# Kernel optimization log

Hardware: AMD Instinct MI355X
Metric: run time of the kernel (lower is better)

The kernel has to match this reference:

```python
import jax, jax.numpy as jnp
import numpy as np
from jax import lax

B, C, D, H, W = 2, 256, 32, 64, 192
TRAIN_W = 640
DISPS = np.arange(D, dtype=np.float32) * 0.01  # norm_disp_range


def conv1x1(x, w, b):
    # x [B,Cin,H,W], w [Cout,Cin]
    return jnp.einsum('bchw,oc->bohw', x, w) + b[None, :, None, None]


def conv3x3(x, w, b):
    y = lax.conv_general_dilated(x, w, (1, 1), 'SAME',
                                 dimension_numbers=('NCHW', 'OIHW', 'NCHW'))
    return y + b[None, :, None, None]


def warp_volume(x, shift_px):
    """Horizontal bilinear warp with border clamp for each disparity.
    x [B,Cc,H,W], shift_px [B,D] (pixel shift) -> [B,Cc,D,H,W]."""
    Wd = x.shape[3]
    j = jnp.arange(Wd, dtype=x.dtype)
    src = jnp.clip(j[None, None, :] + shift_px[:, :, None], 0.0, Wd - 1.0)  # [B,D,W]
    x0 = jnp.floor(src).astype(jnp.int32)
    x1 = jnp.minimum(x0 + 1, Wd - 1)
    frac = src - x0.astype(src.dtype)  # [B,D,W]

    def one(xb, i0, i1, fb):
        g0 = xb[:, :, i0]  # [Cc,H,D,W]
        g1 = xb[:, :, i1]
        out = g0 * (1.0 - fb) + g1 * fb
        return out.transpose(0, 2, 1, 3)  # [Cc,D,H,W]

    return jax.vmap(one)(x, x0, x1, frac)


def setup_inputs() -> dict:
    key = jax.random.key(0)
    ks = jax.random.split(key, 16)
    f32 = jnp.float32
    inp = {
        't_feat': jax.random.normal(ks[0], (B, C, H, W), f32),
        's_feat': jax.random.normal(ks[1], (B, C, H, W), f32),
        'directs': jnp.ones((B, 1, 1, 1), f32),
        'qw': jax.random.normal(ks[2], (C // 4, C), f32) * 0.05,
        'qb': jax.random.normal(ks[3], (C // 4,), f32) * 0.05,
        'kw': jax.random.normal(ks[4], (C // 4, C), f32) * 0.05,
        'kb': jax.random.normal(ks[5], (C // 4,), f32) * 0.05,
        'vw': jax.random.normal(ks[6], (C // 4, C), f32) * 0.05,
        'vb': jax.random.normal(ks[7], (C // 4,), f32) * 0.05,
        'p1w': jax.random.normal(ks[8], (C // 4, C // 2, 3, 3), f32) * 0.05,
        'p1b': jax.random.normal(ks[9], (C // 4,), f32) * 0.05,
        'p2w': jax.random.normal(ks[10], (D, C // 4, 3, 3), f32) * 0.05,
        'p2b': jax.random.normal(ks[11], (D,), f32) * 0.05,
        'rw': jax.random.normal(ks[12], (C, C + D), f32) * 0.05,
        'rb': jax.random.normal(ks[13], (C,), f32) * 0.05,
        'img_w': TRAIN_W,
    }
    return inp


def reference(t_feat, s_feat, directs, qw, qb, kw, kb, vw, vb,
              p1w, p1b, p2w, p2b, rw, rb, img_w):
    rel_scale = (TRAIN_W / img_w) if img_w != TRAIN_W else 1.0
    q = conv1x1(t_feat, qw, qb)  # [B,C/4,H,W]
    k = conv1x1(s_feat, kw, kb)
    v = conv1x1(s_feat, vw, vb)

    Wd = t_feat.shape[3]
    disps = jnp.asarray(DISPS, t_feat.dtype)
    # normalized shift d*2*rel_scale*directs -> pixels: * (W-1)/2
    shift = disps[None, :] * rel_scale * directs.reshape(-1, 1) * (Wd - 1)  # [B,D]

    wk = warp_volume(k, shift)  # [B,C/4,D,H,W]
    wv = warp_volume(v, shift)

    cq = q.shape[1]
    cost = jnp.einsum('bchw,bcdhw->bdhw', q, wk) / (cq ** 0.5)  # [B,D,H,W]
    norm_cost = jax.nn.softmax(cost, axis=1)
    agg_v = jnp.einsum('bdhw,bcdhw->bchw', norm_cost, wv)  # [B,C/4,H,W]

    h1 = jax.nn.elu(conv3x3(jnp.concatenate([q, agg_v], axis=1), p1w, p1b))
    res_cost = conv3x3(h1, p2w, p2b)  # [B,D,H,W]
    cost = (cost + res_cost) * 0.5
    norm_cost = jax.nn.softmax(cost, axis=1)
    x = jax.nn.elu(conv1x1(jnp.concatenate([t_feat, norm_cost], axis=1), rw, rb))
    return x, cost
```

## Files before the change

kernel.cpp:

```cpp
#include <hip/hip_runtime.h>

#define BB 2
#define CC 256
#define CQ 64
#define DD 32
#define HH 64
#define WW 192
#define HW (HH*WW)
#define NPIX (BB*HW)

typedef __attribute__((ext_vector_type(8))) short bf16x8;
typedef __attribute__((ext_vector_type(4))) float f32x4;

__device__ __forceinline__ float b2f(ushort s){ return __uint_as_float(((uint)s)<<16); }
__device__ __forceinline__ ushort f2b(float f){
    uint u = __float_as_uint(f);
    return (ushort)((u + 0x7fffu + ((u>>16)&1u)) >> 16);
}
__device__ __forceinline__ float eluf(float v){ return v > 0.f ? v : (__expf(v)-1.f); }

__global__ __launch_bounds__(256) void k_prep_w(
    const float* __restrict__ qw, const float* __restrict__ qb,
    const float* __restrict__ kw, const float* __restrict__ kb,
    const float* __restrict__ vw, const float* __restrict__ vb,
    const float* __restrict__ p1w, const float* __restrict__ p2w,
    const float* __restrict__ rw,
    ushort* __restrict__ Wqkv, float* __restrict__ bqkv,
    ushort* __restrict__ A1, ushort* __restrict__ A2, ushort* __restrict__ Ar)
{
    int id = blockIdx.x*256 + threadIdx.x;
    if (id < 49152) {
        int o = id / 256, c = id % 256;
        float v = (o<64)? qw[o*256+c] : (o<128)? kw[(o-64)*256+c] : vw[(o-128)*256+c];
        Wqkv[id] = f2b(v);
    } else if (id < 49344) {
        int o = id - 49152;
        bqkv[o] = (o<64)? qb[o] : (o<128)? kb[o-64] : vb[o-128];
    } else if (id < 49344+73728) {
        int i = id - 49344;
        int o = i/1152, r = i%1152, t = r/128, ci = r%128;
        A1[i] = f2b(p1w[(size_t)(o*128+ci)*9 + t]);
    } else if (id < 49344+73728+18432) {
        int i = id - (49344+73728);
        int o = i/576, r = i%576, t = r/64, ci = r%64;
        A2[i] = f2b(p2w[(size_t)(o*64+ci)*9 + t]);
    } else if (id < 49344+73728+18432+73728) {
        int i = id - (49344+73728+18432);
        Ar[i] = f2b(rw[i]);
    }
}

__global__ __launch_bounds__(256) void g_qkv(
    const float* __restrict__ t_feat, const float* __restrict__ s_feat,
    const ushort* __restrict__ Wqkv, const float* __restrict__ bqkv,
    ushort* __restrict__ X1, ushort* __restrict__ VbT)
{
    __shared__ ushort sT[32*264];
    __shared__ ushort sS[32*264];
    int tid = threadIdx.x;
    int bid = blockIdx.x;
    int tile = (bid & 7)*96 + (bid >> 3);
    int p0 = tile * 32;
    int b0  = p0 / HW;
    int pl0 = p0 % HW;

    for (int i = tid; i < 1024; i += 256){
        int px = i & 31, c8 = i >> 5;
        const float* pt = t_feat + ((size_t)(b0*CC + c8*8))*HW + pl0 + px;
        const float* ps = s_feat + ((size_t)(b0*CC + c8*8))*HW + pl0 + px;
        uint ut[4], us[4];
        #pragma unroll
        for (int j2=0;j2<4;++j2){
            ut[j2] = (uint)f2b(pt[(size_t)(2*j2)*HW]) | ((uint)f2b(pt[(size_t)(2*j2+1)*HW])<<16);
            us[j2] = (uint)f2b(ps[(size_t)(2*j2)*HW]) | ((uint)f2b(ps[(size_t)(2*j2+1)*HW])<<16);
        }
        uint4 qt; qt.x=ut[0]; qt.y=ut[1]; qt.z=ut[2]; qt.w=ut[3];
        uint4 qs; qs.x=us[0]; qs.y=us[1]; qs.z=us[2]; qs.w=us[3];
        *(uint4*)&sT[(px*33 + c8)*8] = qt;
        *(uint4*)&sS[(px*33 + c8)*8] = qs;
    }
    __syncthreads();

    int wv = tid >> 6, lane = tid & 63;
    int lm = lane & 15, lk = lane >> 4;
    f32x4 acc[3][2];
    #pragma unroll
    for (int g=0;g<3;++g){ acc[g][0]=(f32x4){0.f,0.f,0.f,0.f}; acc[g][1]=(f32x4){0.f,0.f,0.f,0.f}; }
    const ushort* Ap = Wqkv + (size_t)(wv*16 + lm)*CC + lk*8;

    #pragma unroll
    for (int k0=0; k0<CC; k0+=32){
        bf16x8 a0 = *(const bf16x8*)(Ap + k0);
        bf16x8 a1 = *(const bf16x8*)(Ap + 64*CC + k0);
        bf16x8 a2 = *(const bf16x8*)(Ap + 128*CC + k0);
        #pragma unroll
        for (int nt=0; nt<2; ++nt){
            int ch = (nt*16+lm)*33 + (k0>>3) + lk;
            bf16x8 bT = *(const bf16x8*)&sT[ch*8];
            bf16x8 bS = *(const bf16x8*)&sS[ch*8];
            acc[0][nt] = __builtin_amdgcn_mfma_f32_16x16x32_bf16(a0, bT, acc[0][nt], 0,0,0);
            acc[1][nt] = __builtin_amdgcn_mfma_f32_16x16x32_bf16(a1, bS, acc[1][nt], 0,0,0);
            acc[2][nt] = __builtin_amdgcn_mfma_f32_16x16x32_bf16(a2, bS, acc[2][nt], 0,0,0);
        }
    }
    int ol = wv*16 + lk*4;
    #pragma unroll
    for (int nt=0; nt<2; ++nt){
        int p = p0 + nt*16 + lm;
        {
            int ob = ol;
            uint u0 = (uint)f2b(acc[0][nt][0]+bqkv[ob])   | ((uint)f2b(acc[0][nt][1]+bqkv[ob+1])<<16);
            uint u1 = (uint)f2b(acc[0][nt][2]+bqkv[ob+2]) | ((uint)f2b(acc[0][nt][3]+bqkv[ob+3])<<16);
            *(uint2*)(X1 + (size_t)p*128 + ol) = make_uint2(u0, u1);
        }
        {
            int ob = 64 + ol;
            uint u0 = (uint)f2b(acc[1][nt][0]+bqkv[ob])   | ((uint)f2b(acc[1][nt][1]+bqkv[ob+1])<<16);
            uint u1 = (uint)f2b(acc[1][nt][2]+bqkv[ob+2]) | ((uint)f2b(acc[1][nt][3]+bqkv[ob+3])<<16);
            *(uint2*)(X1 + (size_t)p*128 + 64 + ol) = make_uint2(u0, u1);
        }
        #pragma unroll
        for (int j=0;j<4;++j)
            VbT[(size_t)(ol+j)*NPIX + p] = f2b(acc[2][nt][j] + bqkv[128 + ol + j]);
    }
}

#define BANDC 96
#define STS 36
#define PFS 100
#define VTS2 104
__global__ __launch_bounds__(512) void k_ca(
    const ushort* __restrict__ X1, const ushort* __restrict__ VbT,
    const float* __restrict__ directs, const int* __restrict__ img_w_p,
    float* __restrict__ C1, ushort* __restrict__ Agg)
{
    __shared__ float  sF[BANDC*STS];
    __shared__ ushort sPC[32*VTS2];
    int tid = threadIdx.x;
    int j   = blockIdx.x;
    int r8  = j & 7;
    int kk  = j >> 3;
    int sub = kk % 6;
    int rhi = kk / 6;
    int row = rhi*8 + r8;
    int b   = row >> 6;
    int h   = row & 63;
    int w0  = sub * 32;
    size_t rowbase = (size_t)b*HW + (size_t)h*WW;

    int imw = img_w_p[0];
    float rel = (imw != 640) ? (640.0f/(float)imw) : 1.0f;
    float sf = 0.01f * rel * directs[b] * 191.0f;
    int bl = (sf < 0.f) ? (w0 - 64) : w0;

    int w8 = tid >> 6, lane = tid & 63;
    int lm = lane & 15, lk = lane >> 4;

    {
        int mt = w8 & 1;
        int q  = w0 + mt*16 + lm;
        const ushort* Qp = X1 + (rowbase + q)*128 + lk*8;
        bf16x8 aq0 = *(const bf16x8*)(Qp);
        bf16x8 aq1 = *(const bf16x8*)(Qp + 32);
        for (int nt = (w8 >> 1); nt < 6; nt += 4){
            int xrow = nt*16 + lm;
            int gx = bl + xrow;
            bf16x8 b0 = {0,0,0,0,0,0,0,0}, b1 = {0,0,0,0,0,0,0,0};
            if (gx >= 0 && gx < WW){
                const ushort* Kp = X1 + (rowbase + gx)*128 + 64 + lk*8;
                b0 = *(const bf16x8*)(Kp);
                b1 = *(const bf16x8*)(Kp + 32);
            }
            f32x4 acc = {0.f,0.f,0.f,0.f};
            acc = __builtin_amdgcn_mfma_f32_16x16x32_bf16(aq0, b0, acc, 0,0,0);
            acc = __builtin_amdgcn_mfma_f32_16x16x32_bf16(aq1, b1, acc, 0,0,0);
            *(f32x4*)&sF[xrow*STS + mt*16 + lk*4] = acc;
        }
    }
    __syncthreads();

    int px  = tid >> 4;
    int l16 = tid & 15;
    int w   = w0 + px;
    size_t n = rowbase + w;
    float wf = (float)w;

    float cost[2]; int xi0[2], xi1[2]; float frk[2];
    #pragma unroll
    for (int t=0; t<2; ++t){
        int d = l16*2 + t;
        float srcx = fminf(fmaxf(wf + (float)d*sf, 0.f), 191.0f);
        int x0 = (int)floorf(srcx);
        int x1 = min(x0+1, WW-1);
        float fr = srcx - (float)x0;
        int i0 = min(max(x0 - bl, 0), BANDC-1);
        int i1 = min(max(x1 - bl, 0), BANDC-1);
        xi0[t] = i0; xi1[t] = i1; frk[t] = fr;
        float s0 = sF[i0*STS + px];
        float s1 = sF[i1*STS + px];
        cost[t] = (s0 + fr*(s1-s0)) * 0.125f;
    }
    *(float2*)(C1 + n*DD + l16*2) = make_float2(cost[0], cost[1]);
    float mm = fmaxf(cost[0], cost[1]);
    mm = fmaxf(mm, __shfl_xor(mm, 1));
    mm = fmaxf(mm, __shfl_xor(mm, 2));
    mm = fmaxf(mm, __shfl_xor(mm, 4));
    mm = fmaxf(mm, __shfl_xor(mm, 8));
    float e0 = __expf(cost[0]-mm), e1 = __expf(cost[1]-mm);
    float ss = e0 + e1;
    ss += __shfl_xor(ss, 1);
    ss += __shfl_xor(ss, 2);
    ss += __shfl_xor(ss, 4);
    ss += __shfl_xor(ss, 8);
    float inv = 1.f/ss;
    float p0 = e0*inv, p1 = e1*inv;
    __syncthreads();

    for (int i = tid; i < (32*PFS)/4; i += 512)
        *(f32x4*)&sF[i*4] = (f32x4){0.f,0.f,0.f,0.f};
    __syncthreads();

    {
        float w1a = p0*frk[0], w0a = p0 - w1a;
        float w1b = p1*frk[1], w0b = p1 - w1b;
        atomicAdd(&sF[px*PFS + xi0[0]], w0a);
        atomicAdd(&sF[px*PFS + xi1[0]], w1a);
        atomicAdd(&sF[px*PFS + xi0[1]], w0b);
        atomicAdd(&sF[px*PFS + xi1[1]], w1b);
    }
    __syncthreads();

    {
        int base = l16*6;
        #pragma unroll
        for (int q=0; q<3; ++q){
            float2 v2 = *(const float2*)&sF[px*PFS + base + q*2];
            *(uint*)&sPC[px*VTS2 + base + q*2] = (uint)f2b(v2.x) | ((uint)f2b(v2.y)<<16);
        }
    }
    __syncthreads();

    {
        int mi = w8 & 3;
        int ni = w8 >> 2;
        int c  = mi*16 + lm;
        int wr = ni*16 + lm;
        const ushort* Vp = VbT + (size_t)c*NPIX + rowbase + bl;
        f32x4 acc = {0.f,0.f,0.f,0.f};
        #pragma unroll
        for (int kt=0; kt<3; ++kt){
            int gx = bl + kt*32 + lk*8;
            bf16x8 a = {0,0,0,0,0,0,0,0};
            if (gx >= 0 && gx < WW) a = *(const bf16x8*)(Vp + kt*32 + lk*8);
            bf16x8 bbf = *(const bf16x8*)&sPC[wr*VTS2 + kt*32 + lk*8];
            acc = __builtin_amdgcn_mfma_f32_16x16x32_bf16(a, bbf, acc, 0,0,0);
        }
        uint u0 = (uint)f2b(acc[0]) | ((uint)f2b(acc[1])<<16);
        uint u1 = (uint)f2b(acc[2]) | ((uint)f2b(acc[3])<<16);
        *(uint2*)(Agg + (rowbase + w0 + wr)*64 + mi*16 + lk*4) = make_uint2(u0, u1);
    }
}

__global__ __launch_bounds__(256) void g_conv1(
    const ushort* __restrict__ X1, const ushort* __restrict__ Agg,
    const ushort* __restrict__ A1, const float* __restrict__ p1b,
    ushort* __restrict__ X2)
{
    __shared__ ushort sB[3*16*34*8];
    int tid = threadIdx.x;
    int wv = tid >> 6, lane = tid & 63;
    int lm = lane & 15, lk = lane >> 4;
    int bid = blockIdx.x;
    int tile = (bid & 7)*96 + (bid >> 3);
    int n0 = tile * 32;
    int b  = n0 / HW;
    int pl = n0 % HW;
    int h  = pl / WW, w0 = pl % WW;

    for (int i = tid; i < 1632; i += 256){
        int dh = i / 544, rem2 = i % 544;
        int c16 = rem2 / 34, x = rem2 % 34;
        int hh = h + dh - 1, wx = w0 + x - 1;
        uint4 val = make_uint4(0,0,0,0);
        if (hh >= 0 && hh < HH && wx >= 0 && wx < WW){
            size_t pix = (size_t)b*HW + (size_t)hh*WW + wx;
            val = (c16 < 8) ? *(const uint4*)(X1 + pix*128 + c16*8)
                            : *(const uint4*)(Agg + pix*64 + (c16-8)*8);
        }
        *(uint4*)&sB[((dh*16 + c16)*34 + x)*8] = val;
    }
    __syncthreads();

    int mw = wv & 1, nw = wv >> 1;
    const ushort* Ap = A1 + (size_t)(mw*32 + lm)*1152 + lk*8;
    f32x4 acc0 = {0.f,0.f,0.f,0.f}, acc1 = {0.f,0.f,0.f,0.f};
    int xb = nw*16 + lm;
    #pragma unroll
    for (int t=0; t<9; ++t){
        int dh = t/3, dw = t%3;
        #pragma unroll
        for (int c0=0; c0<128; c0+=32){
            bf16x8 bb = *(const bf16x8*)&sB[((dh*16 + (c0>>3)+lk)*34 + xb + dw)*8];
            bf16x8 a0 = *(const bf16x8*)(Ap + t*128 + c0);
            bf16x8 a1 = *(const bf16x8*)(Ap + (size_t)16*1152 + t*128 + c0);
            acc0 = __builtin_amdgcn_mfma_f32_16x16x32_bf16(a0, bb, acc0, 0,0,0);
            acc1 = __builtin_amdgcn_mfma_f32_16x16x32_bf16(a1, bb, acc1, 0,0,0);
        }
    }
    int pg = n0 + nw*16 + lm;
    int o0 = mw*32 + lk*4;
    {
        uint u0 = (uint)f2b(eluf(acc0[0]+p1b[o0]))   | ((uint)f2b(eluf(acc0[1]+p1b[o0+1]))<<16);
        uint u1 = (uint)f2b(eluf(acc0[2]+p1b[o0+2])) | ((uint)f2b(eluf(acc0[3]+p1b[o0+3]))<<16);
        *(uint2*)(X2 + (size_t)pg*64 + o0) = make_uint2(u0, u1);
        int o1 = o0 + 16;
        uint u2 = (uint)f2b(eluf(acc1[0]+p1b[o1]))   | ((uint)f2b(eluf(acc1[1]+p1b[o1+1]))<<16);
        uint u3 = (uint)f2b(eluf(acc1[2]+p1b[o1+2])) | ((uint)f2b(eluf(acc1[3]+p1b[o1+3]))<<16);
        *(uint2*)(X2 + (size_t)pg*64 + o1) = make_uint2(u2, u3);
    }
}

__global__ __launch_bounds__(256) void g_conv2final(
    const ushort* __restrict__ X2, const ushort* __restrict__ A2,
    const float* __restrict__ p2b, const float* __restrict__ C1,
    const float* __restrict__ t_feat, const ushort* __restrict__ Ar,
    const float* __restrict__ rb,
    float* __restrict__ cost_out, float* __restrict__ xout)
{
    __shared__ ushort sT[32*264];
    __shared__ float  sO[32*36];
    __shared__ ushort sN[32*40];
    ushort* sB = sT;
    int tid = threadIdx.x;
    int wv = tid >> 6, lane = tid & 63;
    int lm = lane & 15, lk = lane >> 4;
    int bid = blockIdx.x;
    int tile = (bid & 7)*96 + (bid >> 3);
    int n0 = tile * 32;
    int b  = n0 / HW;
    int pl = n0 % HW;
    int h  = pl / WW, w0 = pl % WW;

    for (int i = tid; i < 816; i += 256){
        int dh = i / 272, rem2 = i % 272;
        int c16 = rem2 / 34, x = rem2 % 34;
        int hh = h + dh - 1, wx = w0 + x - 1;
        uint4 val = make_uint4(0,0,0,0);
        if (hh >= 0 && hh < HH && wx >= 0 && wx < WW)
            val = *(const uint4*)(X2 + ((size_t)b*HW + (size_t)hh*WW + wx)*64 + c16*8);
        *(uint4*)&sB[((dh*8 + c16)*34 + x)*8] = val;
    }
    __syncthreads();

    {
        int mw = wv & 1, nw = wv >> 1;
        const ushort* Ap = A2 + (size_t)(mw*16 + lm)*576 + lk*8;
        f32x4 acc = {0.f,0.f,0.f,0.f};
        int xb = nw*16 + lm;
        #pragma unroll
        for (int t=0; t<9; ++t){
            int dh = t/3, dw = t%3;
            #pragma unroll
            for (int c0=0; c0<64; c0+=32){
                bf16x8 bb = *(const bf16x8*)&sB[((dh*8 + (c0>>3)+lk)*34 + xb + dw)*8];
                bf16x8 a  = *(const bf16x8*)(Ap + t*64 + c0);
                acc = __builtin_amdgcn_mfma_f32_16x16x32_bf16(a, bb, acc, 0,0,0);
            }
        }
        int pg = n0 + nw*16 + lm;
        int pll = pg % HW;
        int o = mw*16 + lk*4;
        f32x4 cv = *(const f32x4*)(C1 + (size_t)pg*DD + o);
        f32x4 outv;
        #pragma unroll
        for (int j=0;j<4;++j){
            outv[j] = (cv[j] + acc[j] + p2b[o+j]) * 0.5f;
            cost_out[((size_t)(b*DD + o + j))*HW + pll] = outv[j];
        }
        *(f32x4*)&sO[(nw*16 + lm)*36 + o] = outv;
    }
    __syncthreads();

    {
        int px = tid >> 3;
        int g  = tid & 7;
        f32x4 v = *(const f32x4*)&sO[px*36 + g*4];
        float m = fmaxf(fmaxf(v[0],v[1]), fmaxf(v[2],v[3]));
        m = fmaxf(m, __shfl_xor(m, 1));
        m = fmaxf(m, __shfl_xor(m, 2));
        m = fmaxf(m, __shfl_xor(m, 4));
        float e[4]; float s = 0.f;
        #pragma unroll
        for (int j=0;j<4;++j){ e[j] = __expf(v[j]-m); s += e[j]; }
        s += __shfl_xor(s, 1);
        s += __shfl_xor(s, 2);
        s += __shfl_xor(s, 4);
        float invs = 1.f/s;
        uint u0 = (uint)f2b(e[0]*invs) | ((uint)f2b(e[1]*invs)<<16);
        uint u1 = (uint)f2b(e[2]*invs) | ((uint)f2b(e[3]*invs)<<16);
        *(uint2*)&sN[px*40 + g*4] = make_uint2(u0, u1);
    }
    for (int i = tid; i < 1024; i += 256){
        int px = i & 31, c8 = i >> 5;
        const float* pt = t_feat + ((size_t)(b*CC + c8*8))*HW + pl + px;
        uint u[4];
        #pragma unroll
        for (int j2=0;j2<4;++j2)
            u[j2] = (uint)f2b(pt[(size_t)(2*j2)*HW]) | ((uint)f2b(pt[(size_t)(2*j2+1)*HW])<<16);
        uint4 q4; q4.x=u[0]; q4.y=u[1]; q4.z=u[2]; q4.w=u[3];
        *(uint4*)&sT[(px*33 + c8)*8] = q4;
    }
    __syncthreads();

    {
        f32x4 acc[4][2];
        #pragma unroll
        for (int mi=0;mi<4;++mi){ acc[mi][0]=(f32x4){0.f,0.f,0.f,0.f}; acc[mi][1]=(f32x4){0.f,0.f,0.f,0.f}; }
        const ushort* Ap = Ar + (size_t)(wv*64 + lm)*288 + lk*8;

        #pragma unroll
        for (int k0=0; k0<288; k0+=32){
            bf16x8 a[4];
            #pragma unroll
            for (int mi=0;mi<4;++mi) a[mi] = *(const bf16x8*)(Ap + (size_t)mi*16*288 + k0);
            #pragma unroll
            for (int nt=0; nt<2; ++nt){
                int prow = nt*16 + lm;
                bf16x8 bb = (k0 < 256) ? *(const bf16x8*)&sT[(prow*33 + (k0>>3) + lk)*8]
                                       : *(const bf16x8*)&sN[(prow*5 + lk)*8];
                #pragma unroll
                for (int mi=0;mi<4;++mi)
                    acc[mi][nt] = __builtin_amdgcn_mfma_f32_16x16x32_bf16(a[mi], bb, acc[mi][nt], 0,0,0);
            }
        }
        #pragma unroll
        for (int mi=0;mi<4;++mi){
            int o = wv*64 + mi*16 + lk*4;
            #pragma unroll
            for (int nt=0; nt<2; ++nt){
                int p = n0 + nt*16 + lm;
                int bb2 = p / HW, pl2 = p % HW;
                #pragma unroll
                for (int j=0;j<4;++j)
                    xout[((size_t)(bb2*CC + o + j))*HW + pl2] = eluf(acc[mi][nt][j] + rb[o+j]);
            }
        }
    }
}

extern "C" void kernel_launch(void* const* d_in, const int* in_sizes, int n_in,
                              void* d_out, int out_size, void* d_ws, size_t ws_size,
                              hipStream_t stream)
{
    const float* t_feat = (const float*)d_in[0];
    const float* s_feat = (const float*)d_in[1];
    const float* directs= (const float*)d_in[2];
    const float* qw = (const float*)d_in[3];
    const float* qb = (const float*)d_in[4];
    const float* kw = (const float*)d_in[5];
    const float* kb = (const float*)d_in[6];
    const float* vw = (const float*)d_in[7];
    const float* vb = (const float*)d_in[8];
    const float* p1w= (const float*)d_in[9];
    const float* p1b= (const float*)d_in[10];
    const float* p2w= (const float*)d_in[11];
    const float* p2b= (const float*)d_in[12];
    const float* rw = (const float*)d_in[13];
    const float* rb = (const float*)d_in[14];
    const int* img_w= (const int*)d_in[15];

    char* wsb = (char*)d_ws;
    char*  tsreg = wsb + 12582912;
    ushort* X2   = (ushort*)tsreg;
    float*  C1   = (float*)(tsreg + 3145728);
    ushort* Agg  = (ushort*)(tsreg + 6291456);
    ushort* X1   = (ushort*)(wsb + 25165824);
    ushort* VbT  = (ushort*)(wsb + 31457280);
    ushort* Wqkv = (ushort*)(wsb + 34603008);
    float*  bqkv = (float*) (wsb + 34701312);
    ushort* A1   = (ushort*)(wsb + 34702336);
    ushort* A2   = (ushort*)(wsb + 34849792);
    ushort* Ar   = (ushort*)(wsb + 34886656);
    if (ws_size < 35034112) return;

    float* xout     = (float*)d_out;
    float* cost_out = xout + (size_t)BB*CC*HW;

    k_prep_w    <<<841,  256, 0, stream>>>(qw,qb,kw,kb,vw,vb,p1w,p2w,rw,
                                           Wqkv,bqkv,A1,A2,Ar);
    g_qkv       <<<768,  256, 0, stream>>>(t_feat, s_feat, Wqkv, bqkv, X1, VbT);
    k_ca        <<<768,  512, 0, stream>>>(X1, VbT, directs, img_w, C1, Agg);
    g_conv1     <<<768,  256, 0, stream>>>(X1, Agg, A1, p1b, X2);
    g_conv2final<<<768,  256, 0, stream>>>(X2, A2, p2b, C1, t_feat, Ar, rb,
                                           cost_out, xout);
}
```

Before: 96.97 us.

## Shrink cost-aggregation tile to 16 pixels and fuse bf16 conversion into MFMA load

The cost-aggregation kernel now handles 16 pixels per block with 256 threads instead of 32 pixels with 512, doubling the grid to 1536 blocks. The shared probability buffer is zeroed up front, which removes two barriers, and the separate fp32-to-bf16 staging pass is dropped in favour of converting while loading the MFMA B operand. This cuts barriers and shared-memory traffic per block and adds parallelism. In exchange, each block recomputes the 96-wide QK band for half as many pixels, which roughly doubles redundant K loads and MFMA work.

```diff
diff --git a/kernel.cpp b/kernel.cpp
--- a/kernel.cpp
+++ b/kernel.cpp
@@ -126,26 +126,25 @@
 }
 
 #define BANDC 96
-#define STS 36
-#define PFS 100
-#define VTS2 104
-__global__ __launch_bounds__(512) void k_ca(
+#define STS2 20
+#define PFS2 100
+__global__ __launch_bounds__(256) void k_ca(
     const ushort* __restrict__ X1, const ushort* __restrict__ VbT,
     const float* __restrict__ directs, const int* __restrict__ img_w_p,
     float* __restrict__ C1, ushort* __restrict__ Agg)
 {
-    __shared__ float  sF[BANDC*STS];
-    __shared__ ushort sPC[32*VTS2];
+    __shared__ float sS[BANDC*STS2];
+    __shared__ float sPCf[16*PFS2];
     int tid = threadIdx.x;
     int j   = blockIdx.x;
     int r8  = j & 7;
     int kk  = j >> 3;
-    int sub = kk % 6;
-    int rhi = kk / 6;
+    int sub = kk % 12;
+    int rhi = kk / 12;
     int row = rhi*8 + r8;
     int b   = row >> 6;
     int h   = row & 63;
-    int w0  = sub * 32;
+    int w0  = sub * 16;
     size_t rowbase = (size_t)b*HW + (size_t)h*WW;
 
     int imw = img_w_p[0];
@@ -153,17 +152,18 @@
     float sf = 0.01f * rel * directs[b] * 191.0f;
     int bl = (sf < 0.f) ? (w0 - 64) : w0;
 
-    int w8 = tid >> 6, lane = tid & 63;
+    int wv = tid >> 6, lane = tid & 63;
     int lm = lane & 15, lk = lane >> 4;
 
-    {
-        int mt = w8 & 1;
-        int q  = w0 + mt*16 + lm;
-        const ushort* Qp = X1 + (rowbase + q)*128 + lk*8;
+    for (int i = tid; i < 400; i += 256)
+        *(f32x4*)&sPCf[i*4] = (f32x4){0.f,0.f,0.f,0.f};
+
+    {
+        const ushort* Qp = X1 + (rowbase + w0 + lm)*128 + lk*8;
         bf16x8 aq0 = *(const bf16x8*)(Qp);
         bf16x8 aq1 = *(const bf16x8*)(Qp + 32);
-        for (int nt = (w8 >> 1); nt < 6; nt += 4){
-            int xrow = nt*16 + lm;
+        for (int xt = wv; xt < 6; xt += 4){
+            int xrow = xt*16 + lm;
             int gx = bl + xrow;
             bf16x8 b0 = {0,0,0,0,0,0,0,0}, b1 = {0,0,0,0,0,0,0,0};
             if (gx >= 0 && gx < WW){
@@ -174,7 +174,7 @@
             f32x4 acc = {0.f,0.f,0.f,0.f};
             acc = __builtin_amdgcn_mfma_f32_16x16x32_bf16(aq0, b0, acc, 0,0,0);
             acc = __builtin_amdgcn_mfma_f32_16x16x32_bf16(aq1, b1, acc, 0,0,0);
-            *(f32x4*)&sF[xrow*STS + mt*16 + lk*4] = acc;
+            *(f32x4*)&sS[xrow*STS2 + lk*4] = acc;
         }
     }
     __syncthreads();
@@ -196,8 +196,8 @@
         int i0 = min(max(x0 - bl, 0), BANDC-1);
         int i1 = min(max(x1 - bl, 0), BANDC-1);
         xi0[t] = i0; xi1[t] = i1; frk[t] = fr;
-        float s0 = sF[i0*STS + px];
-        float s1 = sF[i1*STS + px];
+        float s0 = sS[i0*STS2 + px];
+        float s1 = sS[i1*STS2 + px];
         cost[t] = (s0 + fr*(s1-s0)) * 0.125f;
     }
     *(float2*)(C1 + n*DD + l16*2) = make_float2(cost[0], cost[1]);
@@ -214,37 +214,19 @@
     ss += __shfl_xor(ss, 8);
     float inv = 1.f/ss;
     float p0 = e0*inv, p1 = e1*inv;
-    __syncthreads();
-
-    for (int i = tid; i < (32*PFS)/4; i += 512)
-        *(f32x4*)&sF[i*4] = (f32x4){0.f,0.f,0.f,0.f};
-    __syncthreads();
-
     {
         float w1a = p0*frk[0], w0a = p0 - w1a;
         float w1b = p1*frk[1], w0b = p1 - w1b;
-        atomicAdd(&sF[px*PFS + xi0[0]], w0a);
-        atomicAdd(&sF[px*PFS + xi1[0]], w1a);
-        atomicAdd(&sF[px*PFS + xi0[1]], w0b);
-        atomicAdd(&sF[px*PFS + xi1[1]], w1b);
-    }
-    __syncthreads();
-
-    {
-        int base = l16*6;
-        #pragma unroll
-        for (int q=0; q<3; ++q){
-            float2 v2 = *(const float2*)&sF[px*PFS + base + q*2];
-            *(uint*)&sPC[px*VTS2 + base + q*2] = (uint)f2b(v2.x) | ((uint)f2b(v2.y)<<16);
-        }
-    }
-    __syncthreads();
-
-    {
-        int mi = w8 & 3;
-        int ni = w8 >> 2;
+        atomicAdd(&sPCf[px*PFS2 + xi0[0]], w0a);
+        atomicAdd(&sPCf[px*PFS2 + xi1[0]], w1a);
+        atomicAdd(&sPCf[px*PFS2 + xi0[1]], w0b);
+        atomicAdd(&sPCf[px*PFS2 + xi1[1]], w1b);
+    }
+    __syncthreads();
+
+    {
+        int mi = wv;
         int c  = mi*16 + lm;
-        int wr = ni*16 + lm;
         const ushort* Vp = VbT + (size_t)c*NPIX + rowbase + bl;
         f32x4 acc = {0.f,0.f,0.f,0.f};
         #pragma unroll
@@ -252,12 +234,19 @@
             int gx = bl + kt*32 + lk*8;
             bf16x8 a = {0,0,0,0,0,0,0,0};
             if (gx >= 0 && gx < WW) a = *(const bf16x8*)(Vp + kt*32 + lk*8);
-            bf16x8 bbf = *(const bf16x8*)&sPC[wr*VTS2 + kt*32 + lk*8];
+            f32x4 v0 = *(const f32x4*)&sPCf[lm*PFS2 + kt*32 + lk*8];
+            f32x4 v1 = *(const f32x4*)&sPCf[lm*PFS2 + kt*32 + lk*8 + 4];
+            bf16x8 bbf;
+            #pragma unroll
+            for (int jj=0;jj<4;++jj){
+                bbf[jj]   = (short)f2b(v0[jj]);
+                bbf[jj+4] = (short)f2b(v1[jj]);
+            }
             acc = __builtin_amdgcn_mfma_f32_16x16x32_bf16(a, bbf, acc, 0,0,0);
         }
         uint u0 = (uint)f2b(acc[0]) | ((uint)f2b(acc[1])<<16);
         uint u1 = (uint)f2b(acc[2]) | ((uint)f2b(acc[3])<<16);
-        *(uint2*)(Agg + (rowbase + w0 + wr)*64 + mi*16 + lk*4) = make_uint2(u0, u1);
+        *(uint2*)(Agg + (rowbase + w0 + lm)*64 + mi*16 + lk*4) = make_uint2(u0, u1);
     }
 }
 
@@ -489,7 +478,7 @@
     k_prep_w    <<<841,  256, 0, stream>>>(qw,qb,kw,kb,vw,vb,p1w,p2w,rw,
                                            Wqkv,bqkv,A1,A2,Ar);
     g_qkv       <<<768,  256, 0, stream>>>(t_feat, s_feat, Wqkv, bqkv, X1, VbT);
-    k_ca        <<<768,  512, 0, stream>>>(X1, VbT, directs, img_w, C1, Agg);
+    k_ca        <<<1536, 256, 0, stream>>>(X1, VbT, directs, img_w, C1, Agg);
     g_conv1     <<<768,  256, 0, stream>>>(X1, Agg, A1, p1b, X2);
     g_conv2final<<<768,  256, 0, stream>>>(X2, A2, p2b, C1, t_feat, Ar, rb,
                                            cost_out, xout);
```

After: 95.55 us. Within noise of the previous version (-1.5%).
